# Optimization experiments

Measured on AMD Instinct MI355X. Metric: run time of the kernel, lower is better.

The kernel has to match this reference:

```python
import jax, jax.numpy as jnp
import numpy as np

EPS = 1e-06


def setup_inputs() -> dict:
    key = jax.random.key(0)
    k1, k2 = jax.random.split(key)
    N, C, H, W = 256, 3, 256, 256
    preds = jax.random.normal(k1, (N, C, H, W), dtype=jnp.float32)
    targets = jax.random.normal(k2, (N, C, H, W), dtype=jnp.float32)
    return {"preds": preds, "targets": targets}


def reference(preds, targets):
    N = preds.shape[0]
    # Flatten to [N, D] as in torch's .view(len, -1)
    Z = targets.reshape(N, -1)  # targets first, matching the torch call order
    B = preds.reshape(N, -1)
    Z_c = Z - jnp.mean(Z, axis=1, keepdims=True)
    B_c = B - jnp.mean(B, axis=1, keepdims=True)
    # Full N x N cross-correlation matrix (faithful to original), then diagonal
    num = jnp.einsum('nd,md->nm', Z_c, B_c)
    Z_norm = jnp.linalg.norm(Z_c, axis=1, keepdims=True)  # [N,1]
    B_norm = jnp.linalg.norm(B_c, axis=1, keepdims=True)  # [N,1]
    denom = Z_norm @ B_norm.T  # [N,N]
    pearson = num / (denom + EPS)
    corr = jnp.diagonal(pearson)  # [N]
    return jnp.mean(corr)  # reduction='mean'
```

## Files before the change

### kernel.cpp

```cpp
#include <hip/hip_runtime.h>
#include <stdint.h>


typedef float f4 __attribute__((ext_vector_type(4)));

constexpr int NROWS  = 256;
constexpr int D      = 3 * 256 * 256;
constexpr int D4     = D / 4;
constexpr int TPB1   = 256;
constexpr int BATCH  = 4;
constexpr int C4     = TPB1 * BATCH;
constexpr int CHUNKS = D4 / C4;
constexpr double EPS = 1e-6;

__device__ __forceinline__ void async_ld16(const void* g, void* l) {
    __builtin_amdgcn_global_load_lds(
        (const __attribute__((address_space(1))) uint32_t*)g,
        (__attribute__((address_space(3))) uint32_t*)l,
        16, 0, 2);
}

__global__ __launch_bounds__(TPB1) void partial_kernel(
        const f4* __restrict__ preds,
        const f4* __restrict__ targets,
        double* __restrict__ partials)
{
    __shared__ f4 sBuf[2][BATCH][TPB1];

    const int  blk   = blockIdx.x;
    const int  row   = blk / CHUNKS;
    const int  chunk = blk % CHUNKS;
    const int  tid   = threadIdx.x;
    const int  w     = tid >> 6;
    const long G     = (long)row * D4 + (long)chunk * C4;

    #pragma unroll
    for (int u = 0; u < BATCH; ++u) {
        const long gi = G + (long)u * TPB1 + tid;
        async_ld16(&preds[gi],   &sBuf[0][u][w * 64]);
        async_ld16(&targets[gi], &sBuf[1][u][w * 64]);
    }
    __syncthreads();

    double sZ = 0.0, sB = 0.0, sZZ = 0.0, sBB = 0.0, sZB = 0.0;
    #pragma unroll
    for (int u = 0; u < BATCH; ++u) {
        const f4 b4 = sBuf[0][u][tid];
        const f4 z4 = sBuf[1][u][tid];
        double z, b;
        z = (double)z4.x; b = (double)b4.x;
        sZ += z; sB += b; sZZ = fma(z,z,sZZ); sBB = fma(b,b,sBB); sZB = fma(z,b,sZB);
        z = (double)z4.y; b = (double)b4.y;
        sZ += z; sB += b; sZZ = fma(z,z,sZZ); sBB = fma(b,b,sBB); sZB = fma(z,b,sZB);
        z = (double)z4.z; b = (double)b4.z;
        sZ += z; sB += b; sZZ = fma(z,z,sZZ); sBB = fma(b,b,sBB); sZB = fma(z,b,sZB);
        z = (double)z4.w; b = (double)b4.w;
        sZ += z; sB += b; sZZ = fma(z,z,sZZ); sBB = fma(b,b,sBB); sZB = fma(z,b,sZB);
    }

    #pragma unroll
    for (int off = 32; off > 0; off >>= 1) {
        sZ  += __shfl_down(sZ,  off);
        sB  += __shfl_down(sB,  off);
        sZZ += __shfl_down(sZZ, off);
        sBB += __shfl_down(sBB, off);
        sZB += __shfl_down(sZB, off);
    }

    constexpr int NWAVES = TPB1 / 64;
    __shared__ double sm[5][NWAVES];
    const int lane = tid & 63;
    if (lane == 0) {
        sm[0][w] = sZ;  sm[1][w] = sB;
        sm[2][w] = sZZ; sm[3][w] = sBB;
        sm[4][w] = sZB;
    }
    __syncthreads();

    if (tid == 0) {
        double* out = partials + (long)blk * 5;
        #pragma unroll
        for (int k = 0; k < 5; ++k)
            out[k] = sm[k][0] + sm[k][1] + sm[k][2] + sm[k][3];
    }
}

__global__ __launch_bounds__(64) void row_reduce_kernel(
        const double* __restrict__ partials, double* __restrict__ rowcorr)
{
    const int row = blockIdx.x;
    const int c   = threadIdx.x;
    double tZ = 0, tB = 0, tZZ = 0, tBB = 0, tZB = 0;
    if (c < CHUNKS) {
        const double* p = partials + ((long)row * CHUNKS + c) * 5;
        tZ = p[0]; tB = p[1]; tZZ = p[2]; tBB = p[3]; tZB = p[4];
    }
    #pragma unroll
    for (int off = 32; off > 0; off >>= 1) {
        tZ  += __shfl_down(tZ,  off);
        tB  += __shfl_down(tB,  off);
        tZZ += __shfl_down(tZZ, off);
        tBB += __shfl_down(tBB, off);
        tZB += __shfl_down(tZB, off);
    }
    if (c == 0) {
        const double invD = 1.0 / (double)D;
        const double num  = tZB - tZ * tB * invD;
        const double varZ = fmax(tZZ - tZ * tZ * invD, 0.0);
        const double varB = fmax(tBB - tB * tB * invD, 0.0);
        const double den  = sqrt(varZ) * sqrt(varB) + EPS;
        rowcorr[row] = num / den;
    }
}

__global__ __launch_bounds__(NROWS) void mean_kernel(
        const double* __restrict__ rowcorr, float* __restrict__ out)
{
    const int tid = threadIdx.x;
    double v = rowcorr[tid];
    #pragma unroll
    for (int off = 32; off > 0; off >>= 1) v += __shfl_down(v, off);

    __shared__ double sm[NROWS / 64];
    const int wave = tid >> 6;
    const int lane = tid & 63;
    if (lane == 0) sm[wave] = v;
    __syncthreads();
    if (tid == 0) {
        double t = 0.0;
        #pragma unroll
        for (int w = 0; w < NROWS / 64; ++w) t += sm[w];
        out[0] = (float)(t / (double)NROWS);
    }
}

extern "C" void kernel_launch(void* const* d_in, const int* in_sizes, int n_in,
                              void* d_out, int out_size, void* d_ws, size_t ws_size,
                              hipStream_t stream) {
    const f4* preds   = (const f4*)d_in[0];
    const f4* targets = (const f4*)d_in[1];
    double* partials = (double*)d_ws;
    double* rowcorr  = partials + (long)NROWS * CHUNKS * 5;
    float*  out      = (float*)d_out;

    hipLaunchKernelGGL(partial_kernel, dim3(NROWS * CHUNKS), dim3(TPB1), 0, stream,
                       preds, targets, partials);
    hipLaunchKernelGGL(row_reduce_kernel, dim3(NROWS), dim3(64), 0, stream,
                       partials, rowcorr);
    hipLaunchKernelGGL(mean_kernel, dim3(1), dim3(NROWS), 0, stream,
                       rowcorr, out);
}
```

Measured before the change: 358.9 us.

## Loop each block over multiple chunks and fuse row-reduce with mean kernel

Replaces one-block-per-chunk launch with 4 blocks per row that each loop over 12 chunks, accumulating in registers and writing fewer partials. Merges the row-reduction and mean kernels into a single one-block finishing kernel. Intends to cut block scheduling, partial writes and launch overhead, but lowers the resident block count and serializes load and compute within each block since there is no double buffering.

```diff
diff --git a/kernel.cpp b/kernel.cpp
--- a/kernel.cpp
+++ b/kernel.cpp
@@ -4,13 +4,14 @@
 
 typedef float f4 __attribute__((ext_vector_type(4)));
 
-constexpr int NROWS  = 256;
-constexpr int D      = 3 * 256 * 256;
-constexpr int D4     = D / 4;
-constexpr int TPB1   = 256;
-constexpr int BATCH  = 4;
-constexpr int C4     = TPB1 * BATCH;
-constexpr int CHUNKS = D4 / C4;
+constexpr int NROWS = 256;
+constexpr int D     = 3 * 256 * 256;
+constexpr int D4    = D / 4;
+constexpr int TPB   = 256;
+constexpr int BATCH = 4;
+constexpr int C4    = TPB * BATCH;
+constexpr int SLOTS = 4;
+constexpr int ITERS = D4 / (SLOTS * C4);
 constexpr double EPS = 1e-6;
 
 __device__ __forceinline__ void async_ld16(const void* g, void* l) {
@@ -20,42 +21,47 @@
         16, 0, 2);
 }
 
-__global__ __launch_bounds__(TPB1) void partial_kernel(
+__global__ __launch_bounds__(TPB) void partial_kernel(
         const f4* __restrict__ preds,
         const f4* __restrict__ targets,
         double* __restrict__ partials)
 {
-    __shared__ f4 sBuf[2][BATCH][TPB1];
+    __shared__ f4 sBuf[2][BATCH][TPB];
 
-    const int  blk   = blockIdx.x;
-    const int  row   = blk / CHUNKS;
-    const int  chunk = blk % CHUNKS;
-    const int  tid   = threadIdx.x;
-    const int  w     = tid >> 6;
-    const long G     = (long)row * D4 + (long)chunk * C4;
-
-    #pragma unroll
-    for (int u = 0; u < BATCH; ++u) {
-        const long gi = G + (long)u * TPB1 + tid;
-        async_ld16(&preds[gi],   &sBuf[0][u][w * 64]);
-        async_ld16(&targets[gi], &sBuf[1][u][w * 64]);
-    }
-    __syncthreads();
+    const int  blk  = blockIdx.x;
+    const int  row  = blk / SLOTS;
+    const int  slot = blk % SLOTS;
+    const int  tid  = threadIdx.x;
+    const int  w    = tid >> 6;
+    const int  lane = tid & 63;
+    const long base0 = (long)row * D4 + (long)slot * (ITERS * C4);
 
     double sZ = 0.0, sB = 0.0, sZZ = 0.0, sBB = 0.0, sZB = 0.0;
-    #pragma unroll
-    for (int u = 0; u < BATCH; ++u) {
-        const f4 b4 = sBuf[0][u][tid];
-        const f4 z4 = sBuf[1][u][tid];
-        double z, b;
-        z = (double)z4.x; b = (double)b4.x;
-        sZ += z; sB += b; sZZ = fma(z,z,sZZ); sBB = fma(b,b,sBB); sZB = fma(z,b,sZB);
-        z = (double)z4.y; b = (double)b4.y;
-        sZ += z; sB += b; sZZ = fma(z,z,sZZ); sBB = fma(b,b,sBB); sZB = fma(z,b,sZB);
-        z = (double)z4.z; b = (double)b4.z;
-        sZ += z; sB += b; sZZ = fma(z,z,sZZ); sBB = fma(b,b,sBB); sZB = fma(z,b,sZB);
-        z = (double)z4.w; b = (double)b4.w;
-        sZ += z; sB += b; sZZ = fma(z,z,sZZ); sBB = fma(b,b,sBB); sZB = fma(z,b,sZB);
+
+    for (int i = 0; i < ITERS; ++i) {
+        const long base = base0 + (long)i * C4;
+        #pragma unroll
+        for (int u = 0; u < BATCH; ++u) {
+            const long gi = base + u * TPB + tid;
+            async_ld16(&preds[gi],   &sBuf[0][u][w * 64]);
+            async_ld16(&targets[gi], &sBuf[1][u][w * 64]);
+        }
+        asm volatile("s_waitcnt vmcnt(0)" ::: "memory");
+
+        #pragma unroll
+        for (int u = 0; u < BATCH; ++u) {
+            const f4 b4 = sBuf[0][u][tid];
+            const f4 z4 = sBuf[1][u][tid];
+            double z, b;
+            z = (double)z4.x; b = (double)b4.x;
+            sZ += z; sB += b; sZZ = fma(z,z,sZZ); sBB = fma(b,b,sBB); sZB = fma(z,b,sZB);
+            z = (double)z4.y; b = (double)b4.y;
+            sZ += z; sB += b; sZZ = fma(z,z,sZZ); sBB = fma(b,b,sBB); sZB = fma(z,b,sZB);
+            z = (double)z4.z; b = (double)b4.z;
+            sZ += z; sB += b; sZZ = fma(z,z,sZZ); sBB = fma(b,b,sBB); sZB = fma(z,b,sZB);
+            z = (double)z4.w; b = (double)b4.w;
+            sZ += z; sB += b; sZZ = fma(z,z,sZZ); sBB = fma(b,b,sBB); sZB = fma(z,b,sZB);
+        }
     }
 
     #pragma unroll
@@ -67,16 +73,13 @@
         sZB += __shfl_down(sZB, off);
     }
 
-    constexpr int NWAVES = TPB1 / 64;
-    __shared__ double sm[5][NWAVES];
-    const int lane = tid & 63;
+    __shared__ double sm[5][TPB / 64];
     if (lane == 0) {
         sm[0][w] = sZ;  sm[1][w] = sB;
         sm[2][w] = sZZ; sm[3][w] = sBB;
         sm[4][w] = sZB;
     }
     __syncthreads();
-
     if (tid == 0) {
         double* out = partials + (long)blk * 5;
         #pragma unroll
@@ -85,48 +88,32 @@
     }
 }
 
-__global__ __launch_bounds__(64) void row_reduce_kernel(
-        const double* __restrict__ partials, double* __restrict__ rowcorr)
+__global__ __launch_bounds__(NROWS) void finish_kernel(
+        const double* __restrict__ partials, float* __restrict__ out)
 {
-    const int row = blockIdx.x;
-    const int c   = threadIdx.x;
+    const int r = threadIdx.x;
     double tZ = 0, tB = 0, tZZ = 0, tBB = 0, tZB = 0;
-    if (c < CHUNKS) {
-        const double* p = partials + ((long)row * CHUNKS + c) * 5;
-        tZ = p[0]; tB = p[1]; tZZ = p[2]; tBB = p[3]; tZB = p[4];
+    #pragma unroll
+    for (int s = 0; s < SLOTS; ++s) {
+        const double* p = partials + ((long)r * SLOTS + s) * 5;
+        tZ += p[0]; tB += p[1]; tZZ += p[2]; tBB += p[3]; tZB += p[4];
     }
-    #pragma unroll
-    for (int off = 32; off > 0; off >>= 1) {
-        tZ  += __shfl_down(tZ,  off);
-        tB  += __shfl_down(tB,  off);
-        tZZ += __shfl_down(tZZ, off);
-        tBB += __shfl_down(tBB, off);
-        tZB += __shfl_down(tZB, off);
-    }
-    if (c == 0) {
-        const double invD = 1.0 / (double)D;
-        const double num  = tZB - tZ * tB * invD;
-        const double varZ = fmax(tZZ - tZ * tZ * invD, 0.0);
-        const double varB = fmax(tBB - tB * tB * invD, 0.0);
-        const double den  = sqrt(varZ) * sqrt(varB) + EPS;
-        rowcorr[row] = num / den;
-    }
-}
+    const double invD = 1.0 / (double)D;
+    const double num  = tZB - tZ * tB * invD;
+    const double varZ = fmax(tZZ - tZ * tZ * invD, 0.0);
+    const double varB = fmax(tBB - tB * tB * invD, 0.0);
+    const double den  = sqrt(varZ) * sqrt(varB) + EPS;
+    double v = num / den;
 
-__global__ __launch_bounds__(NROWS) void mean_kernel(
-        const double* __restrict__ rowcorr, float* __restrict__ out)
-{
-    const int tid = threadIdx.x;
-    double v = rowcorr[tid];
     #pragma unroll
     for (int off = 32; off > 0; off >>= 1) v += __shfl_down(v, off);
 
     __shared__ double sm[NROWS / 64];
-    const int wave = tid >> 6;
-    const int lane = tid & 63;
+    const int wave = r >> 6;
+    const int lane = r & 63;
     if (lane == 0) sm[wave] = v;
     __syncthreads();
-    if (tid == 0) {
+    if (r == 0) {
         double t = 0.0;
         #pragma unroll
         for (int w = 0; w < NROWS / 64; ++w) t += sm[w];
@@ -140,13 +127,10 @@
     const f4* preds   = (const f4*)d_in[0];
     const f4* targets = (const f4*)d_in[1];
     double* partials = (double*)d_ws;
-    double* rowcorr  = partials + (long)NROWS * CHUNKS * 5;
     float*  out      = (float*)d_out;
 
-    hipLaunchKernelGGL(partial_kernel, dim3(NROWS * CHUNKS), dim3(TPB1), 0, stream,
+    hipLaunchKernelGGL(partial_kernel, dim3(NROWS * SLOTS), dim3(TPB), 0, stream,
                        preds, targets, partials);
-    hipLaunchKernelGGL(row_reduce_kernel, dim3(NROWS), dim3(64), 0, stream,
-                       partials, rowcorr);
-    hipLaunchKernelGGL(mean_kernel, dim3(1), dim3(NROWS), 0, stream,
-                       rowcorr, out);
+    hipLaunchKernelGGL(finish_kernel, dim3(1), dim3(NROWS), 0, stream,
+                       partials, out);
 }
```

Result: no change. 359.9 us (+0.3%).
